# Performance work log

Hardware: AMD Instinct MI355X
Metric: run time of the kernel (lower is better)

Reference implementation:

```python
import jax, jax.numpy as jnp
import numpy as np

NU = 100000  # user nodes
NI = 100000  # item nodes
D_IN = 128
D_OUT = 128
E = 800000   # edges per canonical etype


def setup_inputs() -> dict:
    key = jax.random.key(0)
    ks = jax.random.split(key, 14)
    s = 1.0 / np.sqrt(D_IN)
    return {
        "feat_user": jax.random.normal(ks[0], (NU, D_IN), jnp.float32),
        "feat_item": jax.random.normal(ks[1], (NI, D_IN), jnp.float32),
        "W_follows": jax.random.normal(ks[2], (D_OUT, D_IN), jnp.float32) * s,
        "b_follows": jax.random.normal(ks[3], (D_OUT,), jnp.float32) * s,
        "W_rates": jax.random.normal(ks[4], (D_OUT, D_IN), jnp.float32) * s,
        "b_rates": jax.random.normal(ks[5], (D_OUT,), jnp.float32) * s,
        "W_ratedby": jax.random.normal(ks[6], (D_OUT, D_IN), jnp.float32) * s,
        "b_ratedby": jax.random.normal(ks[7], (D_OUT,), jnp.float32) * s,
        "src_follows": jax.random.randint(ks[8], (E,), 0, NU),
        "dst_follows": jax.random.randint(ks[9], (E,), 0, NU),
        "src_rates": jax.random.randint(ks[10], (E,), 0, NU),
        "dst_rates": jax.random.randint(ks[11], (E,), 0, NI),
        "src_ratedby": jax.random.randint(ks[12], (E,), 0, NI),
        "dst_ratedby": jax.random.randint(ks[13], (E,), 0, NU),
    }


def _mean_agg(Wh, src, dst, n_dst):
    # gather transformed src features per edge, segment-mean over dst
    msg = Wh[src]  # [E, D_OUT]
    s = jax.ops.segment_sum(msg, dst, num_segments=n_dst)
    cnt = jax.ops.segment_sum(jnp.ones((dst.shape[0],), Wh.dtype), dst,
                              num_segments=n_dst)
    return s / jnp.maximum(cnt, 1.0)[:, None]  # zero-degree -> 0, like DGL


def reference(feat_user, feat_item, W_follows, b_follows, W_rates, b_rates,
              W_ratedby, b_ratedby, src_follows, dst_follows, src_rates,
              dst_rates, src_ratedby, dst_ratedby):
    # per-etype linear transform of source node features (Wh)
    Wh_f = feat_user @ W_follows.T + b_follows    # user -> user
    Wh_r = feat_user @ W_rates.T + b_rates        # user -> item
    Wh_rb = feat_item @ W_ratedby.T + b_ratedby   # item -> user
    # copy_u/mean per etype, then 'sum' combine across etypes per dst ntype
    h_user = (_mean_agg(Wh_f, src_follows, dst_follows, NU)
              + _mean_agg(Wh_rb, src_ratedby, dst_ratedby, NU))
    h_item = _mean_agg(Wh_r, src_rates, dst_rates, NI)
    return (h_user, h_item)
```

## Files before the change

### kernel.cpp

```cpp
#include <hip/hip_runtime.h>

#define NU 100000
#define NI 100000
#define DF 128
#define CAP 32
#define BCAP 768
#define NBKT 1600
#define CHUNK 4096

typedef __attribute__((ext_vector_type(8))) short bf16x8;
typedef __attribute__((ext_vector_type(4))) float f32x4;

__device__ __forceinline__ unsigned short f2bf(float f) {
    unsigned u = __float_as_uint(f);
    return (unsigned short)((u + 0x7fffu + ((u >> 16) & 1u)) >> 16);
}
__device__ __forceinline__ float bflo(unsigned v) { return __uint_as_float(v << 16); }
__device__ __forceinline__ float bfhi(unsigned v) { return __uint_as_float(v & 0xffff0000u); }

__global__ void wcvt_kernel(const float* __restrict__ W0,
                            const float* __restrict__ W1,
                            const float* __restrict__ W2,
                            unsigned short* __restrict__ out,
                            int* __restrict__ bcnt)
{
    const int i = blockIdx.x * 256 + threadIdx.x;
    if (i < 3 * 16384) {
        const float* src = (i < 16384) ? W0 : ((i < 32768) ? W1 : W2);
        out[i] = f2bf(src[i & 16383]);
    }
    if (i < 3 * NBKT * 16) bcnt[i] = 0;
}

__device__ __forceinline__ void stage_a(const float* __restrict__ A,
                                        int rowbase, int M,
                                        unsigned short* __restrict__ lds, int tid)
{
#pragma unroll
    for (int it = 0; it < 16; ++it) {
        const int idx = it * 256 + tid;
        const int row = idx >> 5;
        const int c4  = idx & 31;
        const int rr  = min(rowbase + row, M - 1);
        const float4 f = *(const float4*)(A + (size_t)rr * DF + c4 * 4);
        ushort4 h;
        h.x = f2bf(f.x); h.y = f2bf(f.y); h.z = f2bf(f.z); h.w = f2bf(f.w);
        *(ushort4*)((char*)lds + ((row * 256 + c4 * 8) ^ ((row & 7) << 4))) = h;
    }
}

__device__ __forceinline__ void frag_from_lds(const unsigned short* __restrict__ lds,
                                              int wv, int q, int n,
                                              bf16x8 afrag[2][4])
{
#pragma unroll
    for (int t = 0; t < 2; ++t) {
        const int row = wv * 32 + t * 16 + n;
#pragma unroll
        for (int s = 0; s < 4; ++s)
            afrag[t][s] = *(const bf16x8*)((const char*)lds +
                ((row * 256 + q * 16 + s * 64) ^ ((row & 7) << 4)));
    }
}

__device__ __forceinline__ void mat_pass(const bf16x8 afrag[2][4],
                                         const unsigned short* __restrict__ Wbp,
                                         const float* __restrict__ bias,
                                         unsigned short* __restrict__ ot,
                                         int wv, int q, int n)
{
#pragma unroll 1
    for (int c = 0; c < 8; ++c) {
        const unsigned short* wp = Wbp + (size_t)(c * 16 + n) * DF + q * 8;
        bf16x8 bfrag[4];
#pragma unroll
        for (int s = 0; s < 4; ++s)
            bfrag[s] = *(const bf16x8*)(wp + s * 32);

        f32x4 acc0 = {0.f, 0.f, 0.f, 0.f};
        f32x4 acc1 = {0.f, 0.f, 0.f, 0.f};
#pragma unroll
        for (int s = 0; s < 4; ++s) {
            acc0 = __builtin_amdgcn_mfma_f32_16x16x32_bf16(afrag[0][s], bfrag[s], acc0, 0, 0, 0);
            acc1 = __builtin_amdgcn_mfma_f32_16x16x32_bf16(afrag[1][s], bfrag[s], acc1, 0, 0, 0);
        }

        const float bv = bias[c * 16 + n];
        const int col2 = (c * 16 + n) * 2;
#pragma unroll
        for (int i = 0; i < 4; ++i) {
            const int r0 = wv * 32 + q * 4 + i;
            const int swz = (r0 & 7) << 4;
            *(unsigned short*)((char*)ot + ((r0 * 256 + col2) ^ swz))        = f2bf(acc0[i] + bv);
            *(unsigned short*)((char*)ot + (((r0 + 16) * 256 + col2) ^ swz)) = f2bf(acc1[i] + bv);
        }
    }
}

__device__ __forceinline__ void flush_tile(const unsigned short* __restrict__ ot,
                                           unsigned short* __restrict__ Wh,
                                           int rowbase, int M, int tid)
{
    __syncthreads();
#pragma unroll
    for (int it = 0; it < 8; ++it) {
        const int chunk = it * 256 + tid;
        const int row = chunk >> 4;
        const int lbyte = chunk * 16;
        const uint4 v = *(const uint4*)((const char*)ot + (lbyte ^ ((row & 7) << 4)));
        if (rowbase + row < M)
            *(uint4*)((char*)Wh + (size_t)(rowbase + row) * 256 + (lbyte & 255)) = v;
    }
    __syncthreads();
}

__global__ __launch_bounds__(256)
void gemm3_kernel(const float* __restrict__ Au, const float* __restrict__ Ai,
                  const unsigned short* __restrict__ Wb,
                  const float* __restrict__ b_f, const float* __restrict__ b_r,
                  const float* __restrict__ b_rb,
                  unsigned short* __restrict__ Wh_f,
                  unsigned short* __restrict__ Wh_r,
                  unsigned short* __restrict__ Wh_rb, int M)
{
    __shared__ unsigned short lds[128 * 128];
    const int tid  = threadIdx.x;
    const int lane = tid & 63;
    const int wv   = tid >> 6;
    const int q    = lane >> 4;
    const int n    = lane & 15;
    const int rowbase = blockIdx.x * 128;

    bf16x8 afrag[2][4];
    stage_a(Au, rowbase, M, lds, tid);
    __syncthreads();
    frag_from_lds(lds, wv, q, n, afrag);
    __syncthreads();
    mat_pass(afrag, Wb,             b_f, lds, wv, q, n);
    flush_tile(lds, Wh_f, rowbase, M, tid);
    mat_pass(afrag, Wb + 2 * 16384, b_r, lds, wv, q, n);
    flush_tile(lds, Wh_r, rowbase, M, tid);

    stage_a(Ai, rowbase, M, lds, tid);
    __syncthreads();
    frag_from_lds(lds, wv, q, n, afrag);
    __syncthreads();
    mat_pass(afrag, Wb + 16384,     b_rb, lds, wv, q, n);
    flush_tile(lds, Wh_rb, rowbase, M, tid);
}

__global__ __launch_bounds__(256)
void bin3_kernel(const int* __restrict__ src0, const int* __restrict__ dst0, int n0, int nb0,
                 const int* __restrict__ src1, const int* __restrict__ dst1, int n1, int nb1,
                 const int* __restrict__ src2, const int* __restrict__ dst2, int n2,
                 int* __restrict__ bcnt, unsigned* __restrict__ pairs)
{
    __shared__ int hist[NBKT];
    const int tid = threadIdx.x;
    int b = blockIdx.x, e;
    const int* src; const int* dst; int n;
    if (b < nb0)            { e = 0; src = src0; dst = dst0; n = n0; }
    else if (b < nb0 + nb1) { b -= nb0; e = 1; src = src1; dst = dst1; n = n1; }
    else                    { b -= nb0 + nb1; e = 2; src = src2; dst = dst2; n = n2; }
    const int base = b * CHUNK;
    int* bc = bcnt + e * NBKT * 16;
    unsigned* pr = pairs + (size_t)e * NBKT * BCAP;

    for (int j = tid; j < NBKT; j += 256) hist[j] = 0;
    __syncthreads();

    unsigned pk[16];
    int meta[16];
#pragma unroll
    for (int k = 0; k < 16; ++k) {
        const int i = base + k * 256 + tid;
        if (i < n) {
            const unsigned d = (unsigned)dst[i];
            const unsigned s = (unsigned)src[i];
            pk[k] = (s << 6) | (d & 63u);
            const int p = atomicAdd(&hist[d >> 6], 1);
            meta[k] = (int)((d >> 6) << 16) | p;
        } else meta[k] = -1;
    }
    __syncthreads();
    for (int j = tid; j < NBKT; j += 256) {
        const int c = hist[j];
        hist[j] = (c > 0) ? atomicAdd(&bc[j * 16], c) : 0;
    }
    __syncthreads();
#pragma unroll
    for (int k = 0; k < 16; ++k) {
        if (meta[k] >= 0) {
            const int bkt = meta[k] >> 16;
            const int p = hist[bkt] + (meta[k] & 0xffff);
            if (p < BCAP) pr[(size_t)bkt * BCAP + p] = pk[k];
        }
    }
}

__device__ __forceinline__ void accum8(const uint4 u, float acc[8]) {
    acc[0] += bflo(u.x); acc[1] += bfhi(u.x);
    acc[2] += bflo(u.y); acc[3] += bfhi(u.y);
    acc[4] += bflo(u.z); acc[5] += bfhi(u.z);
    acc[6] += bflo(u.w); acc[7] += bfhi(u.w);
}

__device__ __forceinline__ void gather_q(const unsigned short* __restrict__ Wh,
                                         int s, int d, int dmax,
                                         int selbase, int qh, int c16,
                                         float acc[8])
{
    for (int j = 0; j < dmax; j += 4) {
        const int e0 = j + qh;
        const int e1 = j + 2 + qh;
        const int id0 = __shfl(s, selbase + e0, 64);
        const int id1 = __shfl(s, selbase + e1, 64);
        if (e0 < d) accum8(*((const uint4*)(Wh + (size_t)id0 * DF) + c16), acc);
        if (e1 < d) accum8(*((const uint4*)(Wh + (size_t)id1 * DF) + c16), acc);
    }
}

__global__ __launch_bounds__(256, 8)
void bagg_kernel(const unsigned short* __restrict__ Wh_f,
                 const unsigned short* __restrict__ Wh_rb,
                 const unsigned short* __restrict__ Wh_r,
                 const int* __restrict__ bcnt, const unsigned* __restrict__ pairs,
                 float* __restrict__ out_user, float* __restrict__ out_item)
{
    __shared__ int cntA[64], cntB[64];
    __shared__ unsigned slotA[64 * CAP], slotB[64 * CAP];
    const int tid = threadIdx.x;
    const bool user = (blockIdx.x & 1) == 0;
    const int bkt = blockIdx.x >> 1;

    if (tid < 64) { cntA[tid] = 0; cntB[tid] = 0; }
    __syncthreads();

    const int wv = tid >> 6, lane = tid & 63;
    const int c16 = lane & 15;
    const int qh = (lane >> 4) & 1;
    const int h = lane >> 5;
    const int selbase = lane & 32;

    if (user) {
        const int nf  = min(bcnt[0 * NBKT * 16 + bkt * 16], BCAP);
        const int nrb = min(bcnt[1 * NBKT * 16 + bkt * 16], BCAP);
        const unsigned* prf  = pairs + (size_t)bkt * BCAP;
        const unsigned* prrb = pairs + (size_t)NBKT * BCAP + (size_t)bkt * BCAP;
        for (int i = tid; i < nf; i += 256) {
            const unsigned v = prf[i];
            const int dl = v & 63;
            const int p = atomicAdd(&cntA[dl], 1);
            if (p < CAP) slotA[dl * CAP + p] = v >> 6;
        }
        for (int i = tid; i < nrb; i += 256) {
            const unsigned v = prrb[i];
            const int dl = v & 63;
            const int p = atomicAdd(&cntB[dl], 1);
            if (p < CAP) slotB[dl * CAP + p] = v >> 6;
        }
        __syncthreads();

        for (int t = 0; t < 8; ++t) {
            const int dl = wv * 16 + t * 2 + h;
            const int node = bkt * 64 + dl;
            const int degf  = cntA[dl];
            const int degrb = cntB[dl];
            const int sf  = (int)slotA[dl * CAP + (lane & 31)];
            const int srb = (int)slotB[dl * CAP + (lane & 31)];
            const int df  = min(degf, CAP);
            const int drb = min(degrb, CAP);
            const int dfm  = max(df,  __shfl_xor(df, 32, 64));
            const int drbm = max(drb, __shfl_xor(drb, 32, 64));

            float acc[8];
#pragma unroll
            for (int k = 0; k < 8; ++k) acc[k] = 0.f;
            gather_q(Wh_f, sf, df, dfm, selbase, qh, c16, acc);
            const float invf = degf > 0 ? 1.f / (float)degf : 0.f;
            float res[8];
#pragma unroll
            for (int k = 0; k < 8; ++k) { res[k] = acc[k] * invf; acc[k] = 0.f; }

            gather_q(Wh_rb, srb, drb, drbm, selbase, qh, c16, acc);
            const float invrb = degrb > 0 ? 1.f / (float)degrb : 0.f;
#pragma unroll
            for (int k = 0; k < 8; ++k) {
                res[k] += acc[k] * invrb;
                res[k] += __shfl_xor(res[k], 16, 64);
            }
            if (!(lane & 16) && node < NU) {
                float* op = out_user + (size_t)node * DF + c16 * 8;
                float4 o0 = {res[0], res[1], res[2], res[3]};
                float4 o1 = {res[4], res[5], res[6], res[7]};
                *(float4*)op = o0;
                *((float4*)op + 1) = o1;
            }
        }
    } else {
        const int nr = min(bcnt[2 * NBKT * 16 + bkt * 16], BCAP);
        const unsigned* prr = pairs + 2 * (size_t)NBKT * BCAP + (size_t)bkt * BCAP;
        for (int i = tid; i < nr; i += 256) {
            const unsigned v = prr[i];
            const int dl = v & 63;
            const int p = atomicAdd(&cntA[dl], 1);
            if (p < CAP) slotA[dl * CAP + p] = v >> 6;
        }
        __syncthreads();

        for (int t = 0; t < 8; ++t) {
            const int dl = wv * 16 + t * 2 + h;
            const int node = bkt * 64 + dl;
            const int degr = cntA[dl];
            const int sr = (int)slotA[dl * CAP + (lane & 31)];
            const int dr = min(degr, CAP);
            const int drm = max(dr, __shfl_xor(dr, 32, 64));

            float acc[8];
#pragma unroll
            for (int k = 0; k < 8; ++k) acc[k] = 0.f;
            gather_q(Wh_r, sr, dr, drm, selbase, qh, c16, acc);
            const float invr = degr > 0 ? 1.f / (float)degr : 0.f;
            float res[8];
#pragma unroll
            for (int k = 0; k < 8; ++k) {
                res[k] = acc[k] * invr;
                res[k] += __shfl_xor(res[k], 16, 64);
            }
            if (!(lane & 16) && node < NI) {
                float* op = out_item + (size_t)node * DF + c16 * 8;
                float4 o0 = {res[0], res[1], res[2], res[3]};
                float4 o1 = {res[4], res[5], res[6], res[7]};
                *(float4*)op = o0;
                *((float4*)op + 1) = o1;
            }
        }
    }
}

extern "C" void kernel_launch(void* const* d_in, const int* in_sizes, int n_in,
                              void* d_out, int out_size, void* d_ws,
                              size_t ws_size, hipStream_t stream)
{
    const float* feat_user = (const float*)d_in[0];
    const float* feat_item = (const float*)d_in[1];
    const float* W_f  = (const float*)d_in[2];
    const float* b_f  = (const float*)d_in[3];
    const float* W_r  = (const float*)d_in[4];
    const float* b_r  = (const float*)d_in[5];
    const float* W_rb = (const float*)d_in[6];
    const float* b_rb = (const float*)d_in[7];
    const int* src_f  = (const int*)d_in[8];
    const int* dst_f  = (const int*)d_in[9];
    const int* src_r  = (const int*)d_in[10];
    const int* dst_r  = (const int*)d_in[11];
    const int* src_rb = (const int*)d_in[12];
    const int* dst_rb = (const int*)d_in[13];
    const int Ef  = in_sizes[8];
    const int Er  = in_sizes[10];
    const int Erb = in_sizes[12];

    float* out_user = (float*)d_out;
    float* out_item = (float*)d_out + (size_t)NU * DF;

    char* p = (char*)d_ws;
    unsigned short* Wh_f  = (unsigned short*)p;  p += (size_t)NU * DF * 2;
    unsigned short* Wh_rb = (unsigned short*)p;  p += (size_t)NI * DF * 2;
    unsigned short* Wh_r  = (unsigned short*)p;  p += (size_t)NU * DF * 2;
    unsigned* pairs = (unsigned*)p;  p += 3 * (size_t)NBKT * BCAP * 4;
    int* bcnt = (int*)p;             p += 3 * (size_t)NBKT * 16 * 4;
    unsigned short* Wb = (unsigned short*)p;

    wcvt_kernel<<<300, 256, 0, stream>>>(W_f, W_rb, W_r, Wb, bcnt);

    gemm3_kernel<<<(NU + 127) / 128, 256, 0, stream>>>(
        feat_user, feat_item, Wb, b_f, b_r, b_rb, Wh_f, Wh_r, Wh_rb, NU);

    const int nb_f  = (Ef  + CHUNK - 1) / CHUNK;
    const int nb_rb = (Erb + CHUNK - 1) / CHUNK;
    const int nb_r  = (Er  + CHUNK - 1) / CHUNK;
    bin3_kernel<<<nb_f + nb_rb + nb_r, 256, 0, stream>>>(
        src_f,  dst_f,  Ef,  nb_f,
        src_rb, dst_rb, Erb, nb_rb,
        src_r,  dst_r,  Er,  bcnt, pairs);

    const int nbu = (NU + 63) / 64;
    bagg_kernel<<<2 * nbu, 256, 0, stream>>>(
        Wh_f, Wh_rb, Wh_r, bcnt, pairs, out_user, out_item);
}
```

Before: 423.1 us.

## Gather rows with a full wave per node and branch-free zero-row padding

Restructures the aggregation so each wave handles one destination node, with every lane loading 4 bytes of each neighbour row. Edges that fall outside the real degree read from an added zero sentinel row instead of branching. The f and rb gathers are interleaved with 4 or 8 loads in flight, and the cross-lane shuffle reduction is dropped. User and item blocks are now split into contiguous ranges rather than interleaved. The cost is narrower 4-byte loads per lane in place of 16-byte loads, extra memory traffic for the padded sentinel reads, and slightly larger workspace buffers.

```diff
diff --git a/kernel.cpp b/kernel.cpp
--- a/kernel.cpp
+++ b/kernel.cpp
@@ -10,6 +10,7 @@
 
 typedef __attribute__((ext_vector_type(8))) short bf16x8;
 typedef __attribute__((ext_vector_type(4))) float f32x4;
+typedef __attribute__((ext_vector_type(2))) float f32x2;
 
 __device__ __forceinline__ unsigned short f2bf(float f) {
     unsigned u = __float_as_uint(f);
@@ -22,7 +23,10 @@
                             const float* __restrict__ W1,
                             const float* __restrict__ W2,
                             unsigned short* __restrict__ out,
-                            int* __restrict__ bcnt)
+                            int* __restrict__ bcnt,
+                            unsigned short* __restrict__ Wh_f,
+                            unsigned short* __restrict__ Wh_rb,
+                            unsigned short* __restrict__ Wh_r)
 {
     const int i = blockIdx.x * 256 + threadIdx.x;
     if (i < 3 * 16384) {
@@ -30,6 +34,10 @@
         out[i] = f2bf(src[i & 16383]);
     }
     if (i < 3 * NBKT * 16) bcnt[i] = 0;
+    if (i < 3 * DF) {
+        unsigned short* zp = (i < DF) ? Wh_f : ((i < 2 * DF) ? Wh_rb : Wh_r);
+        zp[(size_t)NU * DF + (i & (DF - 1))] = 0;
+    }
 }
 
 __device__ __forceinline__ void stage_a(const float* __restrict__ A,
@@ -198,49 +206,24 @@
     }
 }
 
-__device__ __forceinline__ void accum8(const uint4 u, float acc[8]) {
-    acc[0] += bflo(u.x); acc[1] += bfhi(u.x);
-    acc[2] += bflo(u.y); acc[3] += bfhi(u.y);
-    acc[4] += bflo(u.z); acc[5] += bfhi(u.z);
-    acc[6] += bflo(u.w); acc[7] += bfhi(u.w);
-}
-
-__device__ __forceinline__ void gather_q(const unsigned short* __restrict__ Wh,
-                                         int s, int d, int dmax,
-                                         int selbase, int qh, int c16,
-                                         float acc[8])
-{
-    for (int j = 0; j < dmax; j += 4) {
-        const int e0 = j + qh;
-        const int e1 = j + 2 + qh;
-        const int id0 = __shfl(s, selbase + e0, 64);
-        const int id1 = __shfl(s, selbase + e1, 64);
-        if (e0 < d) accum8(*((const uint4*)(Wh + (size_t)id0 * DF) + c16), acc);
-        if (e1 < d) accum8(*((const uint4*)(Wh + (size_t)id1 * DF) + c16), acc);
-    }
-}
-
 __global__ __launch_bounds__(256, 8)
 void bagg_kernel(const unsigned short* __restrict__ Wh_f,
                  const unsigned short* __restrict__ Wh_rb,
                  const unsigned short* __restrict__ Wh_r,
                  const int* __restrict__ bcnt, const unsigned* __restrict__ pairs,
-                 float* __restrict__ out_user, float* __restrict__ out_item)
+                 float* __restrict__ out_user, float* __restrict__ out_item,
+                 int nbu)
 {
     __shared__ int cntA[64], cntB[64];
     __shared__ unsigned slotA[64 * CAP], slotB[64 * CAP];
     const int tid = threadIdx.x;
-    const bool user = (blockIdx.x & 1) == 0;
-    const int bkt = blockIdx.x >> 1;
+    const bool user = (blockIdx.x < nbu);
+    const int bkt = user ? blockIdx.x : blockIdx.x - nbu;
 
     if (tid < 64) { cntA[tid] = 0; cntB[tid] = 0; }
     __syncthreads();
 
     const int wv = tid >> 6, lane = tid & 63;
-    const int c16 = lane & 15;
-    const int qh = (lane >> 4) & 1;
-    const int h = lane >> 5;
-    const int selbase = lane & 32;
 
     if (user) {
         const int nf  = min(bcnt[0 * NBKT * 16 + bkt * 16], BCAP);
@@ -261,41 +244,39 @@
         }
         __syncthreads();
 
-        for (int t = 0; t < 8; ++t) {
-            const int dl = wv * 16 + t * 2 + h;
+        for (int t = 0; t < 16; ++t) {
+            const int dl = wv * 16 + t;
             const int node = bkt * 64 + dl;
+            if (node >= NU) break;
             const int degf  = cntA[dl];
             const int degrb = cntB[dl];
-            const int sf  = (int)slotA[dl * CAP + (lane & 31)];
-            const int srb = (int)slotB[dl * CAP + (lane & 31)];
             const int df  = min(degf, CAP);
             const int drb = min(degrb, CAP);
-            const int dfm  = max(df,  __shfl_xor(df, 32, 64));
-            const int drbm = max(drb, __shfl_xor(drb, 32, 64));
-
-            float acc[8];
-#pragma unroll
-            for (int k = 0; k < 8; ++k) acc[k] = 0.f;
-            gather_q(Wh_f, sf, df, dfm, selbase, qh, c16, acc);
-            const float invf = degf > 0 ? 1.f / (float)degf : 0.f;
-            float res[8];
-#pragma unroll
-            for (int k = 0; k < 8; ++k) { res[k] = acc[k] * invf; acc[k] = 0.f; }
-
-            gather_q(Wh_rb, srb, drb, drbm, selbase, qh, c16, acc);
+            const int dmax = max(df, drb);
+            const unsigned* slf = &slotA[dl * CAP];
+            const unsigned* slb = &slotB[dl * CAP];
+
+            f32x2 af = {0.f, 0.f}, ab = {0.f, 0.f};
+            for (int j = 0; j < dmax; j += 4) {
+                unsigned uf[4], ub[4];
+#pragma unroll
+                for (int k = 0; k < 4; ++k) {
+                    const int e = j + k;
+                    const int idf = (e < df)  ? (int)slf[e & (CAP - 1)] : NU;
+                    const int idb = (e < drb) ? (int)slb[e & (CAP - 1)] : NU;
+                    uf[k] = *((const unsigned*)(Wh_f  + (size_t)idf * DF) + lane);
+                    ub[k] = *((const unsigned*)(Wh_rb + (size_t)idb * DF) + lane);
+                }
+#pragma unroll
+                for (int k = 0; k < 4; ++k) {
+                    af += (f32x2){bflo(uf[k]), bfhi(uf[k])};
+                    ab += (f32x2){bflo(ub[k]), bfhi(ub[k])};
+                }
+            }
+            const float invf  = degf  > 0 ? 1.f / (float)degf  : 0.f;
             const float invrb = degrb > 0 ? 1.f / (float)degrb : 0.f;
-#pragma unroll
-            for (int k = 0; k < 8; ++k) {
-                res[k] += acc[k] * invrb;
-                res[k] += __shfl_xor(res[k], 16, 64);
-            }
-            if (!(lane & 16) && node < NU) {
-                float* op = out_user + (size_t)node * DF + c16 * 8;
-                float4 o0 = {res[0], res[1], res[2], res[3]};
-                float4 o1 = {res[4], res[5], res[6], res[7]};
-                *(float4*)op = o0;
-                *((float4*)op + 1) = o1;
-            }
+            const f32x2 r = af * (f32x2){invf, invf} + ab * (f32x2){invrb, invrb};
+            *(float2*)(out_user + (size_t)node * DF + lane * 2) = make_float2(r.x, r.y);
         }
     } else {
         const int nr = min(bcnt[2 * NBKT * 16 + bkt * 16], BCAP);
@@ -308,32 +289,30 @@
         }
         __syncthreads();
 
-        for (int t = 0; t < 8; ++t) {
-            const int dl = wv * 16 + t * 2 + h;
+        for (int t = 0; t < 16; ++t) {
+            const int dl = wv * 16 + t;
             const int node = bkt * 64 + dl;
+            if (node >= NI) break;
             const int degr = cntA[dl];
-            const int sr = (int)slotA[dl * CAP + (lane & 31)];
             const int dr = min(degr, CAP);
-            const int drm = max(dr, __shfl_xor(dr, 32, 64));
-
-            float acc[8];
-#pragma unroll
-            for (int k = 0; k < 8; ++k) acc[k] = 0.f;
-            gather_q(Wh_r, sr, dr, drm, selbase, qh, c16, acc);
+            const unsigned* slr = &slotA[dl * CAP];
+
+            f32x2 ar = {0.f, 0.f};
+            for (int j = 0; j < dr; j += 8) {
+                unsigned ur[8];
+#pragma unroll
+                for (int k = 0; k < 8; ++k) {
+                    const int e = j + k;
+                    const int idr = (e < dr) ? (int)slr[e & (CAP - 1)] : NU;
+                    ur[k] = *((const unsigned*)(Wh_r + (size_t)idr * DF) + lane);
+                }
+#pragma unroll
+                for (int k = 0; k < 8; ++k)
+                    ar += (f32x2){bflo(ur[k]), bfhi(ur[k])};
+            }
             const float invr = degr > 0 ? 1.f / (float)degr : 0.f;
-            float res[8];
-#pragma unroll
-            for (int k = 0; k < 8; ++k) {
-                res[k] = acc[k] * invr;
-                res[k] += __shfl_xor(res[k], 16, 64);
-            }
-            if (!(lane & 16) && node < NI) {
-                float* op = out_item + (size_t)node * DF + c16 * 8;
-                float4 o0 = {res[0], res[1], res[2], res[3]};
-                float4 o1 = {res[4], res[5], res[6], res[7]};
-                *(float4*)op = o0;
-                *((float4*)op + 1) = o1;
-            }
+            const f32x2 r = ar * (f32x2){invr, invr};
+            *(float2*)(out_item + (size_t)node * DF + lane * 2) = make_float2(r.x, r.y);
         }
     }
 }
@@ -364,14 +343,16 @@
     float* out_item = (float*)d_out + (size_t)NU * DF;
 
     char* p = (char*)d_ws;
-    unsigned short* Wh_f  = (unsigned short*)p;  p += (size_t)NU * DF * 2;
-    unsigned short* Wh_rb = (unsigned short*)p;  p += (size_t)NI * DF * 2;
-    unsigned short* Wh_r  = (unsigned short*)p;  p += (size_t)NU * DF * 2;
+    const size_t whsz = ((size_t)NU + 1) * DF * 2;
+    unsigned short* Wh_f  = (unsigned short*)p;  p += whsz;
+    unsigned short* Wh_rb = (unsigned short*)p;  p += whsz;
+    unsigned short* Wh_r  = (unsigned short*)p;  p += whsz;
     unsigned* pairs = (unsigned*)p;  p += 3 * (size_t)NBKT * BCAP * 4;
     int* bcnt = (int*)p;             p += 3 * (size_t)NBKT * 16 * 4;
     unsigned short* Wb = (unsigned short*)p;
 
-    wcvt_kernel<<<300, 256, 0, stream>>>(W_f, W_rb, W_r, Wb, bcnt);
+    wcvt_kernel<<<300, 256, 0, stream>>>(W_f, W_rb, W_r, Wb, bcnt,
+                                         Wh_f, Wh_rb, Wh_r);
 
     gemm3_kernel<<<(NU + 127) / 128, 256, 0, stream>>>(
         feat_user, feat_item, Wb, b_f, b_r, b_rb, Wh_f, Wh_r, Wh_rb, NU);
@@ -385,6 +366,7 @@
         src_r,  dst_r,  Er,  bcnt, pairs);
 
     const int nbu = (NU + 63) / 64;
-    bagg_kernel<<<2 * nbu, 256, 0, stream>>>(
-        Wh_f, Wh_rb, Wh_r, bcnt, pairs, out_user, out_item);
-}
+    const int nbi = (NI + 63) / 64;
+    bagg_kernel<<<nbu + nbi, 256, 0, stream>>>(
+        Wh_f, Wh_rb, Wh_r, bcnt, pairs, out_user, out_item, nbu);
+}
```

Result: faster. 412.9 us (-2.4%).
